# Optimization experiments

Hardware: AMD Instinct MI355X
Metric: run time of the kernel (lower is better)

## Reference

```python
import jax, jax.numpy as jnp
import numpy as np

B = 64
E = 512          # latent_size / h_dim
H = 8            # num_heads
D = E // H       # head_dim
MAX_AGENTS = 254 # max(agents_per_sample) for the deterministic counts below
NEG = -1e9


def setup_inputs() -> dict:
    key = jax.random.key(0)
    k_x, k_wi, k_bi, k_wo, k_bo = jax.random.split(key, 5)
    # deterministic variable agent counts in [128, 254]; sum == 11531, max == 254
    agents = jnp.array([128 + (3 * i) % 129 for i in range(B)], dtype=jnp.int32)
    total = 11531
    att_in = jax.random.normal(k_x, (total, E), dtype=jnp.float32)
    # nn.MultiheadAttention params: packed in-proj [3E, E] + bias, out-proj [E, E] + bias
    w_in = jax.random.normal(k_wi, (3 * E, E), dtype=jnp.float32) * 0.02
    b_in = jax.random.normal(k_bi, (3 * E,), dtype=jnp.float32) * 0.02
    w_out = jax.random.normal(k_wo, (E, E), dtype=jnp.float32) * 0.02
    b_out = jax.random.normal(k_bo, (E,), dtype=jnp.float32) * 0.02
    return {"att_in": att_in, "w_in": w_in, "b_in": b_in,
            "w_out": w_out, "b_out": b_out, "agents_per_sample": agents}


def reference(att_in, w_in, b_in, w_out, b_out, agents_per_sample):
    S = MAX_AGENTS
    # scatter packed rows into padded [B, S, E] via a clipped gather (jit-safe)
    offsets = jnp.cumsum(agents_per_sample) - agents_per_sample      # [B]
    pos = jnp.arange(S, dtype=jnp.int32)
    mask = pos[None, :] < agents_per_sample[:, None]                 # [B, S] valid
    idx = jnp.clip(offsets[:, None] + pos[None, :], 0, att_in.shape[0] - 1)
    padded = jnp.where(mask[..., None], att_in[idx], 0.0)            # [B, S, E]

    # fused QKV projection (torch packed in_proj), dropout disabled (eval)
    qkv = padded @ w_in.T + b_in                                     # [B, S, 3E]
    q, k, v = jnp.split(qkv, 3, axis=-1)
    q = q.reshape(B, S, H, D)
    k = k.reshape(B, S, H, D)
    v = v.reshape(B, S, H, D)

    scores = jnp.einsum('bqhd,bkhd->bhqk', q, k) * (D ** -0.5)      # [B, H, S, S]
    scores = jnp.where(mask[:, None, None, :], scores, NEG)          # key_padding_mask
    attn = jax.nn.softmax(scores, axis=-1)
    ctx = jnp.einsum('bhqk,bkhd->bqhd', attn, v).reshape(B, S, E)
    out = ctx @ w_out.T + b_out                                      # [B, S, E]
    # torch returns only valid rows per sample; zero the padded rows instead
    return out * mask[..., None]
```

## Files before the change

### kernel.cpp

```cpp
#include <hip/hip_runtime.h>
#include <hip/hip_bf16.h>

typedef __attribute__((ext_vector_type(8))) short bf16x8;
typedef __attribute__((ext_vector_type(4))) float f32x4;
typedef __attribute__((ext_vector_type(4))) int i32x4;
typedef __attribute__((ext_vector_type(4))) unsigned short u16x4;
typedef __attribute__((ext_vector_type(2))) unsigned ui2;
typedef __attribute__((ext_vector_type(4))) float fl4;

struct __attribute__((packed)) u16x4u { u16x4 v; };

__device__ __forceinline__ f32x4 mfma16(bf16x8 a, bf16x8 b, f32x4 c) {
    return __builtin_amdgcn_mfma_f32_16x16x32_bf16(a, b, c, 0, 0, 0);
}

__device__ __forceinline__ unsigned short f2b(float f) {
    unsigned u = __float_as_uint(f);
    unsigned r = (u + 0x7FFF + ((u >> 16) & 1)) >> 16;
    return (unsigned short)r;
}

__device__ __forceinline__ int bsearch_off(const int* s_off, int m) {
    int lo = 0, hi = 63;
    while (lo < hi) {
        int mid = (lo + hi + 1) >> 1;
        if (s_off[mid] <= m) lo = mid; else hi = mid - 1;
    }
    return lo;
}

__device__ __forceinline__ void gld_lds16(const __hip_bfloat16* g, __hip_bfloat16* l) {
    __builtin_amdgcn_global_load_lds(
        (const __attribute__((address_space(1))) void*)g,
        (__attribute__((address_space(3))) void*)l,
        16, 0, 0);
}

__global__ void k_prep(const unsigned short* __restrict__ src,
                       const void* __restrict__ b_in, const void* __restrict__ b_out,
                       const int* __restrict__ agents,
                       int* __restrict__ flag, int* __restrict__ offs,
                       float* __restrict__ bfi, float* __restrict__ bfo) {
    __shared__ int sh[256];
    __shared__ int sa[64];
    __shared__ int sflag;
    int tid = threadIdx.x;
    int h = 0;
    for (int i = tid; i < 16384; i += 256) {
        unsigned e = (src[i] >> 7) & 0xFF;
        if (e == 0xFF) h = 1;
    }
    sh[tid] = h;
    if (tid < 64) sa[tid] = agents[tid];
    __syncthreads();
    if (tid < 64) {
        int v = sh[tid] | sh[tid + 64] | sh[tid + 128] | sh[tid + 192];
        unsigned long long m = __ballot(v != 0);
        if (tid == 0) { flag[0] = (m != 0) ? 1 : 0; sflag = (m != 0) ? 1 : 0; }
        int ex = 0;
        for (int i = 0; i < 64; ++i) { int w = sa[i]; if (i < tid) ex += w; }
        offs[tid] = ex;
        if (tid == 63) offs[64] = ex + sa[63];
    }
    __syncthreads();
    int f = sflag;
    for (int i = tid; i < 1536; i += 256)
        bfi[i] = f ? ((const float*)b_in)[i]
                   : __bfloat162float(((const __hip_bfloat16*)b_in)[i]);
    for (int i = tid; i < 512; i += 256)
        bfo[i] = f ? ((const float*)b_out)[i]
                   : __bfloat162float(((const __hip_bfloat16*)b_out)[i]);
}

__global__ void k_cast_all(const void* __restrict__ sA, unsigned short* __restrict__ dA, int nA,
                           const void* __restrict__ sWi, unsigned short* __restrict__ dWi, int nWi,
                           const void* __restrict__ sWo, unsigned short* __restrict__ dWo, int nWo,
                           const int* __restrict__ flag) {
    int i = (blockIdx.x * 256 + threadIdx.x) * 4;
    const void* src; unsigned short* dst; int k;
    if (i < nA)            { src = sA;  dst = dA;  k = i; }
    else if (i < nA + nWi) { src = sWi; dst = dWi; k = i - nA; }
    else if (i < nA + nWi + nWo) { src = sWo; dst = dWo; k = i - nA - nWi; }
    else return;
    u16x4 o;
    if (flag[0]) {
        fl4 v = *(const fl4*)((const float*)src + k);
        o[0] = f2b(v[0]); o[1] = f2b(v[1]); o[2] = f2b(v[2]); o[3] = f2b(v[3]);
    } else {
        o = *(const u16x4*)((const unsigned short*)src + k);
    }
    *(u16x4*)(dst + k) = o;
}

template<int LDA, bool MROWS>
__device__ __forceinline__ void gemm_core(
    const __hip_bfloat16* __restrict__ A,
    const __hip_bfloat16* __restrict__ W,
    int m0, int n0, int total,
    __hip_bfloat16* As, __hip_bfloat16* Ws,
    f32x4 acc[4][4], int tid)
{
    int lane = tid & 63, quad = lane >> 4, c = lane & 15;
    int wave = tid >> 6;
    int wr = wave >> 1, wc = wave & 1;

    const __hip_bfloat16* gA[4];
    const __hip_bfloat16* gW[4];
    __hip_bfloat16* lA[4];
    __hip_bfloat16* lW[4];
#pragma unroll
    for (int j = 0; j < 4; ++j) {
        int L = j * 256 + tid;
        int row = L >> 3;
        int gseg = (L & 7) ^ (row & 7);
        int ar = m0 + row; if (ar > total - 1) ar = total - 1;
        gA[j] = A + (size_t)ar * LDA + gseg * 8;
        gW[j] = W + (size_t)(n0 + row) * 512 + gseg * 8;
        lA[j] = As + (size_t)(j * 256 + wave * 64) * 8;
        lW[j] = Ws + (size_t)(j * 256 + wave * 64) * 8;
    }

#pragma unroll
    for (int j = 0; j < 4; ++j) gld_lds16(gA[j], lA[j]);
#pragma unroll
    for (int j = 0; j < 4; ++j) gld_lds16(gW[j], lW[j]);

#pragma unroll
    for (int s = 0; s < 8; ++s) {
        const int cur = s & 1;
        const int nxt = cur ^ 1;
        if (s < 7) {
            int k0 = (s + 1) * 64;
#pragma unroll
            for (int j = 0; j < 4; ++j) gld_lds16(gA[j] + k0, lA[j] + nxt * (128 * 64));
#pragma unroll
            for (int j = 0; j < 4; ++j) gld_lds16(gW[j] + k0, lW[j] + nxt * (128 * 64));
            asm volatile("s_waitcnt vmcnt(8)" ::: "memory");
        } else {
            asm volatile("s_waitcnt vmcnt(0)" ::: "memory");
        }
        __builtin_amdgcn_s_barrier();
        const __hip_bfloat16* Ab = As + cur * (128 * 64);
        const __hip_bfloat16* Wb = Ws + cur * (128 * 64);
#pragma unroll
        for (int h = 0; h < 2; ++h) {
            bf16x8 af[4], wf[4];
#pragma unroll
            for (int t = 0; t < 4; ++t) {
                int rowa = wr * 64 + t * 16 + c;
                int rowb = wc * 64 + t * 16 + c;
                int ks = quad + 4 * h;
                af[t] = *(const bf16x8*)(Ab + (size_t)rowa * 64 + ((ks ^ (rowa & 7)) * 8));
                wf[t] = *(const bf16x8*)(Wb + (size_t)rowb * 64 + ((ks ^ (rowb & 7)) * 8));
            }
#pragma unroll
            for (int i = 0; i < 4; ++i)
#pragma unroll
                for (int j = 0; j < 4; ++j)
                    acc[i][j] = MROWS ? mfma16(af[i], wf[j], acc[i][j])
                                      : mfma16(wf[j], af[i], acc[i][j]);
        }
        if (s < 7) __builtin_amdgcn_s_barrier();
    }
}

template<bool MROWS>
__device__ __forceinline__ void gemm256_core(
    const __hip_bfloat16* __restrict__ A,
    const __hip_bfloat16* __restrict__ W,
    int m0, int n0, int total,
    __hip_bfloat16* As, __hip_bfloat16* Ws,
    f32x4 acc[8][4], int tid)
{
    int lane = tid & 63, quad = lane >> 4, c = lane & 15;
    int wave = tid >> 6;
    int wm = wave >> 2, wn = wave & 3;

    const __hip_bfloat16* gA[4];
    const __hip_bfloat16* gW[4];
    __hip_bfloat16* lA[4];
    __hip_bfloat16* lW[4];
#pragma unroll
    for (int j = 0; j < 4; ++j) {
        int L = j * 512 + tid;
        int row = L >> 3;
        int gseg = (L & 7) ^ (row & 7);
        int ar = m0 + row; if (ar > total - 1) ar = total - 1;
        gA[j] = A + (size_t)ar * 512 + gseg * 8;
        gW[j] = W + (size_t)(n0 + row) * 512 + gseg * 8;
        lA[j] = As + (size_t)(j * 512 + wave * 64) * 8;
        lW[j] = Ws + (size_t)(j * 512 + wave * 64) * 8;
    }

#pragma unroll
    for (int j = 0; j < 4; ++j) gld_lds16(gA[j], lA[j]);
#pragma unroll
    for (int j = 0; j < 4; ++j) gld_lds16(gW[j], lW[j]);

#pragma unroll
    for (int s = 0; s < 8; ++s) {
        const int cur = s & 1;
        const int nxt = cur ^ 1;
        if (s < 7) {
            int k0 = (s + 1) * 64;
#pragma unroll
            for (int j = 0; j < 4; ++j) gld_lds16(gA[j] + k0, lA[j] + nxt * (256 * 64));
#pragma unroll
            for (int j = 0; j < 4; ++j) gld_lds16(gW[j] + k0, lW[j] + nxt * (256 * 64));
            asm volatile("s_waitcnt vmcnt(8)" ::: "memory");
        } else {
            asm volatile("s_waitcnt vmcnt(0)" ::: "memory");
        }
        __builtin_amdgcn_s_barrier();
        const __hip_bfloat16* Ab = As + cur * (256 * 64);
        const __hip_bfloat16* Wb = Ws + cur * (256 * 64);
#pragma unroll
        for (int h = 0; h < 2; ++h) {
            bf16x8 af[8], wf[4];
            int ks = quad + 4 * h;
#pragma unroll
            for (int t = 0; t < 8; ++t) {
                int rowa = wm * 128 + t * 16 + c;
                af[t] = *(const bf16x8*)(Ab + (size_t)rowa * 64 + ((ks ^ (rowa & 7)) * 8));
            }
#pragma unroll
            for (int t = 0; t < 4; ++t) {
                int rowb = wn * 64 + t * 16 + c;
                wf[t] = *(const bf16x8*)(Wb + (size_t)rowb * 64 + ((ks ^ (rowb & 7)) * 8));
            }
#pragma unroll
            for (int i = 0; i < 8; ++i)
#pragma unroll
                for (int j = 0; j < 4; ++j)
                    acc[i][j] = MROWS ? mfma16(af[i], wf[j], acc[i][j])
                                      : mfma16(wf[j], af[i], acc[i][j]);
        }
        if (s < 7) __builtin_amdgcn_s_barrier();
    }
}

__global__ __launch_bounds__(512, 2) void k_qkv(
    const __hip_bfloat16* __restrict__ A,
    const __hip_bfloat16* __restrict__ W,
    const float* __restrict__ bias,
    const int* __restrict__ offs,
    __hip_bfloat16* __restrict__ qP,
    __hip_bfloat16* __restrict__ kP,
    __hip_bfloat16* __restrict__ vT,
    int total)
{
    __shared__ __hip_bfloat16 As[2 * 256 * 64];
    __shared__ __hip_bfloat16 Ws[2 * 256 * 64];
    __shared__ int s_off[65];
    int l = blockIdx.x;
    int rb = l / 6;
    int cb = l - rb * 6;
    int n0 = cb * 256;
    int m0 = rb * 256;
    int tid = threadIdx.x;
    if (tid < 65) s_off[tid] = offs[tid];
    int lane = tid & 63, quad = lane >> 4, c = lane & 15;
    int wave = tid >> 6, wm = wave >> 2, wn = wave & 3;
    f32x4 z = {0.f, 0.f, 0.f, 0.f};
    f32x4 acc[8][4] = {{z,z,z,z},{z,z,z,z},{z,z,z,z},{z,z,z,z},
                       {z,z,z,z},{z,z,z,z},{z,z,z,z},{z,z,z,z}};

    if (n0 < 1024) {
        gemm256_core<false>(A, W, m0, n0, total, As, Ws, acc, tid);
        __hip_bfloat16* dst = (n0 < 512) ? qP : kP;
        int nb = n0 & 511;
        int head = (nb + wn * 64) >> 6;
        fl4 bv4[4];
#pragma unroll
        for (int j = 0; j < 4; ++j)
            bv4[j] = *(const fl4*)&bias[n0 + wn * 64 + j * 16 + quad * 4];
#pragma unroll
        for (int i = 0; i < 8; ++i) {
            int m = m0 + wm * 128 + i * 16 + c;
            if (m >= total) continue;
            int lo = bsearch_off(s_off, m);
            int vs = m - s_off[lo];
            size_t rowp = ((size_t)(lo * 8 + head) * 256 + vs) * 64;
#pragma unroll
            for (int j = 0; j < 4; ++j) {
                int dcol = j * 16 + quad * 4;
                u16x4 o;
#pragma unroll
                for (int r = 0; r < 4; ++r) o[r] = f2b(acc[i][j][r] + bv4[j][r]);
                *(u16x4*)&dst[rowp + dcol] = o;
            }
        }
    } else {
        gemm256_core<true>(A, W, m0, n0, total, As, Ws, acc, tid);
        float bv[4];
#pragma unroll
        for (int j = 0; j < 4; ++j) bv[j] = bias[n0 + wn * 64 + j * 16 + c];
#pragma unroll
        for (int i = 0; i < 8; ++i) {
            int m_base = m0 + wm * 128 + i * 16 + quad * 4;
            if (m_base >= total) continue;
            int lo = bsearch_off(s_off, m_base);
            bool vec = (m_base + 3 < total) && (s_off[lo + 1] > m_base + 3);
            if (vec) {
                int vs = m_base - s_off[lo];
#pragma unroll
                for (int j = 0; j < 4; ++j) {
                    int vc = n0 - 1024 + wn * 64 + j * 16 + c;
                    size_t idx = ((size_t)(lo * 8 + (vc >> 6)) * 64 + (vc & 63)) * 256 + vs;
                    u16x4 o;
#pragma unroll
                    for (int r = 0; r < 4; ++r) o[r] = f2b(acc[i][j][r] + bv[j]);
                    ((u16x4u*)&vT[idx])->v = o;
                }
            } else {
#pragma unroll
                for (int r = 0; r < 4; ++r) {
                    int m = m_base + r;
                    if (m >= total) continue;
                    int lo2 = bsearch_off(s_off, m);
                    int vs2 = m - s_off[lo2];
#pragma unroll
                    for (int j = 0; j < 4; ++j) {
                        int vc = n0 - 1024 + wn * 64 + j * 16 + c;
                        vT[((size_t)(lo2 * 8 + (vc >> 6)) * 64 + (vc & 63)) * 256 + vs2] =
                            __float2bfloat16(acc[i][j][r] + bv[j]);
                    }
                }
            }
        }
    }
}

__global__ __launch_bounds__(256, 2) void k_attn(
    const __hip_bfloat16* __restrict__ qP,
    const __hip_bfloat16* __restrict__ kP,
    const __hip_bfloat16* __restrict__ vT,
    __hip_bfloat16* __restrict__ ctx,
    const int* __restrict__ agents,
    const int* __restrict__ offs)
{
    __shared__ __attribute__((aligned(16))) char Pl[4][16 * 80];
    int bh = blockIdx.x;
    int b = bh >> 3, h = bh & 7;
    int n = agents[b];
    int off = offs[b];
    int qtiles = (n + 15) >> 4;
    int stmax = (qtiles + 1) >> 1;
    int tid = threadIdx.x;
    int wave = tid >> 6, lane = tid & 63, quad = lane >> 4, c = lane & 15;
    const __hip_bfloat16* qbase = qP + (size_t)bh * 256 * 64;
    const __hip_bfloat16* kbase = kP + (size_t)bh * 256 * 64 + quad * 8;
    const __hip_bfloat16* vbase = vT + (size_t)bh * 64 * 256;
    char* Plw = &Pl[wave][0];

    bf16x8 qB[4][2];
    int nt = 0;
#pragma unroll
    for (int t = 0; t < 4; ++t) {
        int qt = wave + 4 * t;
        if (qt < qtiles) {
            nt = t + 1;
            int qr = qt * 16 + c; if (qr > n - 1) qr = n - 1;
            const __hip_bfloat16* qp = qbase + (size_t)qr * 64 + quad * 8;
            qB[t][0] = *(const bf16x8*)qp;
            qB[t][1] = *(const bf16x8*)(qp + 32);
        }
    }

    f32x4 z = {0.f, 0.f, 0.f, 0.f};
    f32x4 O[4][4] = {{z,z,z,z},{z,z,z,z},{z,z,z,z},{z,z,z,z}};
    float sm[4] = {0.f, 0.f, 0.f, 0.f};

    auto LK = [&](int st, bf16x8 kA[2][2], bf16x8 vA[4]) {
        int k0 = st * 32;
#pragma unroll
        for (int ti = 0; ti < 2; ++ti) {
            int kr = k0 + ti * 16 + c; if (kr > n - 1) kr = n - 1;
            const __hip_bfloat16* kp = kbase + (size_t)kr * 64;
            kA[ti][0] = *(const bf16x8*)kp;
            kA[ti][1] = *(const bf16x8*)(kp + 32);
        }
#pragma unroll
        for (int dt = 0; dt < 4; ++dt)
            vA[dt] = *(const bf16x8*)(vbase + (size_t)(dt * 16 + c) * 256 + k0 + quad * 8);
    };

    auto CMP = [&](int st, bf16x8 kA[2][2], bf16x8 vA[4]) {
        int k0 = st * 32;
#pragma unroll
        for (int t = 0; t < 4; ++t) {
            if (t < nt) {
#pragma unroll
                for (int ti = 0; ti < 2; ++ti) {
                    f32x4 s = mfma16(kA[ti][0], qB[t][0], z);
                    s = mfma16(kA[ti][1], qB[t][1], s);
                    int kbase_i = k0 + ti * 16 + quad * 4;
                    float p0 = (kbase_i + 0 < n) ? __expf(s[0] * 0.125f) : 0.f;
                    float p1 = (kbase_i + 1 < n) ? __expf(s[1] * 0.125f) : 0.f;
                    float p2 = (kbase_i + 2 < n) ? __expf(s[2] * 0.125f) : 0.f;
                    float p3 = (kbase_i + 3 < n) ? __expf(s[3] * 0.125f) : 0.f;
                    sm[t] += (p0 + p1) + (p2 + p3);
                    ui2 dw;
                    dw[0] = (unsigned)f2b(p0) | ((unsigned)f2b(p1) << 16);
                    dw[1] = (unsigned)f2b(p2) | ((unsigned)f2b(p3) << 16);
                    *(ui2*)(Plw + c * 80 + ti * 32 + quad * 8) = dw;
                }
                bf16x8 pB = *(const bf16x8*)(Plw + c * 80 + quad * 16);
#pragma unroll
                for (int dt = 0; dt < 4; ++dt)
                    O[t][dt] = mfma16(vA[dt], pB, O[t][dt]);
            }
        }
    };

    bf16x8 kA[2][2], vA[4], kB[2][2], vB[4], kC[2][2], vC[4];
    LK(0, kA, vA);
    if (1 < stmax) LK(1, kB, vB);
    for (int st = 0; st < stmax; st += 3) {
        if (st + 2 < stmax) LK(st + 2, kC, vC);
        CMP(st, kA, vA);
        if (st + 3 < stmax) LK(st + 3, kA, vA);
        if (st + 1 < stmax) CMP(st + 1, kB, vB);
        if (st + 4 < stmax) LK(st + 4, kB, vB);
        if (st + 2 < stmax) CMP(st + 2, kC, vC);
    }

#pragma unroll
    for (int t = 0; t < 4; ++t) {
        if (t < nt) {
            float v = sm[t];
            v += __shfl_xor(v, 16);
            v += __shfl_xor(v, 32);
            float iv = 1.0f / v;
            int q = (wave + 4 * t) * 16 + c;
            if (q < n) {
                size_t row = (size_t)(off + q) * 512 + h * 64;
#pragma unroll
                for (int dt = 0; dt < 4; ++dt) {
                    u16x4 o;
#pragma unroll
                    for (int r = 0; r < 4; ++r) o[r] = f2b(O[t][dt][r] * iv);
                    *(u16x4*)&ctx[row + dt * 16 + quad * 4] = o;
                }
            }
        }
    }
}

__global__ __launch_bounds__(256) void k_out(
    const __hip_bfloat16* __restrict__ A,
    const __hip_bfloat16* __restrict__ W,
    const float* __restrict__ bias,
    const int* __restrict__ offs,
    const int* __restrict__ agents,
    void* __restrict__ out,
    const int* __restrict__ flag,
    int total, int MT)
{
    __shared__ __hip_bfloat16 As[2 * 128 * 64];
    __shared__ __hip_bfloat16 Ws[2 * 128 * 64];
    __shared__ int s_off[65];
    int l = blockIdx.x;
    int MTpad = ((MT + 7) >> 3) << 3;
    int tid = threadIdx.x;
    if (l >= 4 * MTpad) {
        int b = l - 4 * MTpad;
        int n = agents[b];
        int esz = flag[0] ? 4 : 2;
        long long base = ((long long)b * 254 + n) * 512 * esz;
        long long bytes = (long long)(254 - n) * 512 * esz;
        for (long long i = (long long)tid * 16; i < bytes; i += (long long)256 * 16)
            *(i32x4*)((char*)out + base + i) = (i32x4){0, 0, 0, 0};
        return;
    }
    int inner = l >> 3;
    int cb = inner & 3;
    int rb = (l & 7) + 8 * (inner >> 2);
    if (rb >= MT) return;
    int n0 = cb * 128;
    int m0 = rb * 128;
    if (tid < 65) s_off[tid] = offs[tid];
    f32x4 z = {0.f, 0.f, 0.f, 0.f};
    f32x4 acc[4][4] = {{z,z,z,z},{z,z,z,z},{z,z,z,z},{z,z,z,z}};
    gemm_core<512, false>(A, W, m0, n0, total, As, Ws, acc, tid);

    int f32m = flag[0];
    int lane = tid & 63, quad = lane >> 4, c = lane & 15;
    int wave = tid >> 6, wr = wave >> 1, wc = wave & 1;
    fl4 bv4[4];
#pragma unroll
    for (int j = 0; j < 4; ++j)
        bv4[j] = *(const fl4*)&bias[n0 + wc * 64 + j * 16 + quad * 4];
#pragma unroll
    for (int i = 0; i < 4; ++i) {
        int m = m0 + wr * 64 + i * 16 + c;
        if (m >= total) continue;
        int lo = bsearch_off(s_off, m);
        int os_ = m - s_off[lo];
        size_t rowb = ((size_t)(lo * 254 + os_)) * 512;
#pragma unroll
        for (int j = 0; j < 4; ++j) {
            int col0 = n0 + wc * 64 + j * 16 + quad * 4;
            if (f32m) {
                fl4 o;
#pragma unroll
                for (int r = 0; r < 4; ++r) o[r] = acc[i][j][r] + bv4[j][r];
                *(fl4*)&((float*)out)[rowb + col0] = o;
            } else {
                u16x4 o;
#pragma unroll
                for (int r = 0; r < 4; ++r) o[r] = f2b(acc[i][j][r] + bv4[j][r]);
                *(u16x4*)&((__hip_bfloat16*)out)[rowb + col0] = o;
            }
        }
    }
}

extern "C" void kernel_launch(void* const* d_in, const int* in_sizes, int n_in,
                              void* d_out, int out_size, void* d_ws, size_t ws_size,
                              hipStream_t stream) {
    const void* att_in = d_in[0];
    const void* w_in   = d_in[1];
    const void* b_in   = d_in[2];
    const void* w_out  = d_in[3];
    const void* b_out  = d_in[4];
    const int* agents  = (const int*)d_in[5];
    int total = in_sizes[0] / 512;

    char* p = (char*)d_ws;
    int* flag  = (int*)p;                 p += 256;
    int* offs  = (int*)p;                 p += 512;
    float* bfi = (float*)p;               p += 1536 * 4;
    float* bfo = (float*)p;               p += 512 * 4;
    __hip_bfloat16* WinBf  = (__hip_bfloat16*)p;  p += (size_t)1536 * 512 * 2;
    __hip_bfloat16* WoutBf = (__hip_bfloat16*)p;  p += (size_t)512 * 512 * 2;
    __hip_bfloat16* Abf    = (__hip_bfloat16*)p;  p += (size_t)total * 512 * 2;
    __hip_bfloat16* qP     = (__hip_bfloat16*)p;  p += (size_t)512 * 256 * 64 * 2;
    __hip_bfloat16* kP     = (__hip_bfloat16*)p;  p += (size_t)512 * 256 * 64 * 2;
    __hip_bfloat16* vT     = (__hip_bfloat16*)p;  p += (size_t)512 * 64 * 256 * 2;
    __hip_bfloat16* ctx    = (__hip_bfloat16*)p;  p += (size_t)total * 512 * 2;

    int nA = total * 512, nWi = 1536 * 512, nWo = 512 * 512;
    int ntot = nA + nWi + nWo;

    k_prep<<<1, 256, 0, stream>>>((const unsigned short*)att_in, b_in, b_out,
                                  agents, flag, offs, bfi, bfo);
    k_cast_all<<<(ntot / 4 + 255) / 256, 256, 0, stream>>>(
        att_in, (unsigned short*)Abf, nA,
        w_in,   (unsigned short*)WinBf, nWi,
        w_out,  (unsigned short*)WoutBf, nWo, flag);

    int MT = (total + 127) / 128;
    int MTpad = ((MT + 7) / 8) * 8;
    int MT256 = (total + 255) / 256;
    k_qkv<<<6 * MT256, 512, 0, stream>>>(Abf, WinBf, bfi, offs, qP, kP, vT, total);
    k_attn<<<512, 256, 0, stream>>>(qP, kP, vT, ctx, agents, offs);
    k_out<<<4 * MTpad + 64, 256, 0, stream>>>(ctx, WoutBf, bfo, offs, agents,
                                              d_out, flag, total, MT);
}
```

Measured before the change: 190.2 us.

## Split QKV GEMM K-step into two phases, remap XCD blocks, widen out-proj to 8 waves

```diff
diff --git a/kernel.cpp b/kernel.cpp
--- a/kernel.cpp
+++ b/kernel.cpp
@@ -98,32 +98,32 @@
     const __hip_bfloat16* __restrict__ W,
     int m0, int n0, int total,
     __hip_bfloat16* As, __hip_bfloat16* Ws,
-    f32x4 acc[4][4], int tid)
+    f32x4 acc[4][2], int tid)
 {
     int lane = tid & 63, quad = lane >> 4, c = lane & 15;
     int wave = tid >> 6;
-    int wr = wave >> 1, wc = wave & 1;
-
-    const __hip_bfloat16* gA[4];
-    const __hip_bfloat16* gW[4];
-    __hip_bfloat16* lA[4];
-    __hip_bfloat16* lW[4];
-#pragma unroll
-    for (int j = 0; j < 4; ++j) {
-        int L = j * 256 + tid;
+    int wm = wave >> 2, wn = wave & 3;
+
+    const __hip_bfloat16* gA[2];
+    const __hip_bfloat16* gW[2];
+    __hip_bfloat16* lA[2];
+    __hip_bfloat16* lW[2];
+#pragma unroll
+    for (int j = 0; j < 2; ++j) {
+        int L = j * 512 + tid;
         int row = L >> 3;
         int gseg = (L & 7) ^ (row & 7);
         int ar = m0 + row; if (ar > total - 1) ar = total - 1;
         gA[j] = A + (size_t)ar * LDA + gseg * 8;
         gW[j] = W + (size_t)(n0 + row) * 512 + gseg * 8;
-        lA[j] = As + (size_t)(j * 256 + wave * 64) * 8;
-        lW[j] = Ws + (size_t)(j * 256 + wave * 64) * 8;
-    }
-
-#pragma unroll
-    for (int j = 0; j < 4; ++j) gld_lds16(gA[j], lA[j]);
-#pragma unroll
-    for (int j = 0; j < 4; ++j) gld_lds16(gW[j], lW[j]);
+        lA[j] = As + (size_t)(j * 512 + wave * 64) * 8;
+        lW[j] = Ws + (size_t)(j * 512 + wave * 64) * 8;
+    }
+
+#pragma unroll
+    for (int j = 0; j < 2; ++j) gld_lds16(gA[j], lA[j]);
+#pragma unroll
+    for (int j = 0; j < 2; ++j) gld_lds16(gW[j], lW[j]);
 
 #pragma unroll
     for (int s = 0; s < 8; ++s) {
@@ -132,10 +132,10 @@
         if (s < 7) {
             int k0 = (s + 1) * 64;
 #pragma unroll
-            for (int j = 0; j < 4; ++j) gld_lds16(gA[j] + k0, lA[j] + nxt * (128 * 64));
-#pragma unroll
-            for (int j = 0; j < 4; ++j) gld_lds16(gW[j] + k0, lW[j] + nxt * (128 * 64));
-            asm volatile("s_waitcnt vmcnt(8)" ::: "memory");
+            for (int j = 0; j < 2; ++j) gld_lds16(gA[j] + k0, lA[j] + nxt * (128 * 64));
+#pragma unroll
+            for (int j = 0; j < 2; ++j) gld_lds16(gW[j] + k0, lW[j] + nxt * (128 * 64));
+            asm volatile("s_waitcnt vmcnt(4)" ::: "memory");
         } else {
             asm volatile("s_waitcnt vmcnt(0)" ::: "memory");
         }
@@ -144,19 +144,22 @@
         const __hip_bfloat16* Wb = Ws + cur * (128 * 64);
 #pragma unroll
         for (int h = 0; h < 2; ++h) {
-            bf16x8 af[4], wf[4];
+            bf16x8 af[4], wf[2];
+            int ks = quad + 4 * h;
 #pragma unroll
             for (int t = 0; t < 4; ++t) {
-                int rowa = wr * 64 + t * 16 + c;
-                int rowb = wc * 64 + t * 16 + c;
-                int ks = quad + 4 * h;
+                int rowa = wm * 64 + t * 16 + c;
                 af[t] = *(const bf16x8*)(Ab + (size_t)rowa * 64 + ((ks ^ (rowa & 7)) * 8));
+            }
+#pragma unroll
+            for (int t = 0; t < 2; ++t) {
+                int rowb = wn * 32 + t * 16 + c;
                 wf[t] = *(const bf16x8*)(Wb + (size_t)rowb * 64 + ((ks ^ (rowb & 7)) * 8));
             }
 #pragma unroll
             for (int i = 0; i < 4; ++i)
 #pragma unroll
-                for (int j = 0; j < 4; ++j)
+                for (int j = 0; j < 2; ++j)
                     acc[i][j] = MROWS ? mfma16(af[i], wf[j], acc[i][j])
                                       : mfma16(wf[j], af[i], acc[i][j]);
         }
@@ -201,41 +204,52 @@
     for (int s = 0; s < 8; ++s) {
         const int cur = s & 1;
         const int nxt = cur ^ 1;
-        if (s < 7) {
-            int k0 = (s + 1) * 64;
-#pragma unroll
-            for (int j = 0; j < 4; ++j) gld_lds16(gA[j] + k0, lA[j] + nxt * (256 * 64));
-#pragma unroll
-            for (int j = 0; j < 4; ++j) gld_lds16(gW[j] + k0, lW[j] + nxt * (256 * 64));
-            asm volatile("s_waitcnt vmcnt(8)" ::: "memory");
-        } else {
-            asm volatile("s_waitcnt vmcnt(0)" ::: "memory");
-        }
-        __builtin_amdgcn_s_barrier();
         const __hip_bfloat16* Ab = As + cur * (256 * 64);
         const __hip_bfloat16* Wb = Ws + cur * (256 * 64);
 #pragma unroll
-        for (int h = 0; h < 2; ++h) {
-            bf16x8 af[8], wf[4];
-            int ks = quad + 4 * h;
-#pragma unroll
-            for (int t = 0; t < 8; ++t) {
-                int rowa = wm * 128 + t * 16 + c;
-                af[t] = *(const bf16x8*)(Ab + (size_t)rowa * 64 + ((ks ^ (rowa & 7)) * 8));
-            }
-#pragma unroll
-            for (int t = 0; t < 4; ++t) {
-                int rowb = wn * 64 + t * 16 + c;
-                wf[t] = *(const bf16x8*)(Wb + (size_t)rowb * 64 + ((ks ^ (rowb & 7)) * 8));
-            }
-#pragma unroll
-            for (int i = 0; i < 8; ++i)
-#pragma unroll
-                for (int j = 0; j < 4; ++j)
-                    acc[i][j] = MROWS ? mfma16(af[i], wf[j], acc[i][j])
-                                      : mfma16(wf[j], af[i], acc[i][j]);
-        }
-        if (s < 7) __builtin_amdgcn_s_barrier();
+        for (int ph = 0; ph < 2; ++ph) {
+            if (ph == 0)      asm volatile("s_waitcnt vmcnt(2)" ::: "memory");
+            else if (s < 7)   asm volatile("s_waitcnt vmcnt(6)" ::: "memory");
+            else              asm volatile("s_waitcnt vmcnt(0)" ::: "memory");
+            __builtin_amdgcn_s_barrier();
+            if (s < 7) {
+                int k0 = (s + 1) * 64;
+                if (ph == 0) {
+#pragma unroll
+                    for (int j = 0; j < 4; ++j) gld_lds16(gA[j] + k0, lA[j] + nxt * (256 * 64));
+#pragma unroll
+                    for (int j = 0; j < 2; ++j) gld_lds16(gW[j] + k0, lW[j] + nxt * (256 * 64));
+                } else {
+#pragma unroll
+                    for (int j = 2; j < 4; ++j) gld_lds16(gW[j] + k0, lW[j] + nxt * (256 * 64));
+                }
+            }
+#pragma unroll
+            for (int h = 0; h < 2; ++h) {
+                int ks = quad + 4 * h;
+                bf16x8 af[8], wf[2];
+#pragma unroll
+                for (int t = 0; t < 8; ++t) {
+                    int rowa = wm * 128 + t * 16 + c;
+                    af[t] = *(const bf16x8*)(Ab + (size_t)rowa * 64 + ((ks ^ (rowa & 7)) * 8));
+                }
+#pragma unroll
+                for (int t = 0; t < 2; ++t) {
+                    int rowb = ph * 128 + wn * 32 + t * 16 + c;
+                    wf[t] = *(const bf16x8*)(Wb + (size_t)rowb * 64 + ((ks ^ (rowb & 7)) * 8));
+                }
+                __builtin_amdgcn_s_setprio(1);
+#pragma unroll
+                for (int i = 0; i < 8; ++i)
+#pragma unroll
+                    for (int j = 0; j < 2; ++j) {
+                        int jj = ph * 2 + j;
+                        acc[i][jj] = MROWS ? mfma16(af[i], wf[j], acc[i][jj])
+                                           : mfma16(wf[j], af[i], acc[i][jj]);
+                    }
+                __builtin_amdgcn_s_setprio(0);
+            }
+        }
     }
 }
 
@@ -252,9 +266,13 @@
     __shared__ __hip_bfloat16 As[2 * 256 * 64];
     __shared__ __hip_bfloat16 Ws[2 * 256 * 64];
     __shared__ int s_off[65];
-    int l = blockIdx.x;
-    int rb = l / 6;
-    int cb = l - rb * 6;
+    int nwg = gridDim.x;
+    int bid = blockIdx.x;
+    int xcd = bid & 7, idx = bid >> 3;
+    int q = nwg >> 3, r = nwg & 7;
+    int wg = (xcd < r ? xcd * (q + 1) : r * (q + 1) + (xcd - r) * q) + idx;
+    int rb = wg / 6;
+    int cb = wg - rb * 6;
     int n0 = cb * 256;
     int m0 = rb * 256;
     int tid = threadIdx.x;
@@ -269,24 +287,25 @@
         gemm256_core<false>(A, W, m0, n0, total, As, Ws, acc, tid);
         __hip_bfloat16* dst = (n0 < 512) ? qP : kP;
         int nb = n0 & 511;
-        int head = (nb + wn * 64) >> 6;
         fl4 bv4[4];
 #pragma unroll
-        for (int j = 0; j < 4; ++j)
-            bv4[j] = *(const fl4*)&bias[n0 + wn * 64 + j * 16 + quad * 4];
+        for (int jj = 0; jj < 4; ++jj)
+            bv4[jj] = *(const fl4*)&bias[n0 + (jj >> 1) * 128 + wn * 32 + (jj & 1) * 16 + quad * 4];
 #pragma unroll
         for (int i = 0; i < 8; ++i) {
             int m = m0 + wm * 128 + i * 16 + c;
             if (m >= total) continue;
             int lo = bsearch_off(s_off, m);
             int vs = m - s_off[lo];
-            size_t rowp = ((size_t)(lo * 8 + head) * 256 + vs) * 64;
-#pragma unroll
-            for (int j = 0; j < 4; ++j) {
-                int dcol = j * 16 + quad * 4;
+#pragma unroll
+            for (int jj = 0; jj < 4; ++jj) {
+                int ch = jj >> 1, j2 = jj & 1;
+                int head = (nb >> 6) + ch * 2 + (wn >> 1);
+                int dcol = (wn & 1) * 32 + j2 * 16 + quad * 4;
+                size_t rowp = ((size_t)(lo * 8 + head) * 256 + vs) * 64;
                 u16x4 o;
 #pragma unroll
-                for (int r = 0; r < 4; ++r) o[r] = f2b(acc[i][j][r] + bv4[j][r]);
+                for (int r2 = 0; r2 < 4; ++r2) o[r2] = f2b(acc[i][jj][r2] + bv4[jj][r2]);
                 *(u16x4*)&dst[rowp + dcol] = o;
             }
         }
@@ -294,7 +313,8 @@
         gemm256_core<true>(A, W, m0, n0, total, As, Ws, acc, tid);
         float bv[4];
 #pragma unroll
-        for (int j = 0; j < 4; ++j) bv[j] = bias[n0 + wn * 64 + j * 16 + c];
+        for (int jj = 0; jj < 4; ++jj)
+            bv[jj] = bias[n0 + (jj >> 1) * 128 + wn * 32 + (jj & 1) * 16 + c];
 #pragma unroll
         for (int i = 0; i < 8; ++i) {
             int m_base = m0 + wm * 128 + i * 16 + quad * 4;
@@ -304,26 +324,26 @@
             if (vec) {
                 int vs = m_base - s_off[lo];
 #pragma unroll
-                for (int j = 0; j < 4; ++j) {
-                    int vc = n0 - 1024 + wn * 64 + j * 16 + c;
-                    size_t idx = ((size_t)(lo * 8 + (vc >> 6)) * 64 + (vc & 63)) * 256 + vs;
+                for (int jj = 0; jj < 4; ++jj) {
+                    int vc = n0 - 1024 + (jj >> 1) * 128 + wn * 32 + (jj & 1) * 16 + c;
+                    size_t idxv = ((size_t)(lo * 8 + (vc >> 6)) * 64 + (vc & 63)) * 256 + vs;
                     u16x4 o;
 #pragma unroll
-                    for (int r = 0; r < 4; ++r) o[r] = f2b(acc[i][j][r] + bv[j]);
-                    ((u16x4u*)&vT[idx])->v = o;
+                    for (int r2 = 0; r2 < 4; ++r2) o[r2] = f2b(acc[i][jj][r2] + bv[jj]);
+                    ((u16x4u*)&vT[idxv])->v = o;
                 }
             } else {
 #pragma unroll
-                for (int r = 0; r < 4; ++r) {
-                    int m = m_base + r;
+                for (int r2 = 0; r2 < 4; ++r2) {
+                    int m = m_base + r2;
                     if (m >= total) continue;
                     int lo2 = bsearch_off(s_off, m);
                     int vs2 = m - s_off[lo2];
 #pragma unroll
-                    for (int j = 0; j < 4; ++j) {
-                        int vc = n0 - 1024 + wn * 64 + j * 16 + c;
+                    for (int jj = 0; jj < 4; ++jj) {
+                        int vc = n0 - 1024 + (jj >> 1) * 128 + wn * 32 + (jj & 1) * 16 + c;
                         vT[((size_t)(lo2 * 8 + (vc >> 6)) * 64 + (vc & 63)) * 256 + vs2] =
-                            __float2bfloat16(acc[i][j][r] + bv[j]);
+                            __float2bfloat16(acc[i][jj][r2] + bv[jj]);
                     }
                 }
             }
@@ -447,7 +467,7 @@
     }
 }
 
-__global__ __launch_bounds__(256) void k_out(
+__global__ __launch_bounds__(512, 4) void k_out(
     const __hip_bfloat16* __restrict__ A,
     const __hip_bfloat16* __restrict__ W,
     const float* __restrict__ bias,
@@ -469,7 +489,7 @@
         int esz = flag[0] ? 4 : 2;
         long long base = ((long long)b * 254 + n) * 512 * esz;
         long long bytes = (long long)(254 - n) * 512 * esz;
-        for (long long i = (long long)tid * 16; i < bytes; i += (long long)256 * 16)
+        for (long long i = (long long)tid * 16; i < bytes; i += (long long)512 * 16)
             *(i32x4*)((char*)out + base + i) = (i32x4){0, 0, 0, 0};
         return;
     }
@@ -481,26 +501,26 @@
     int m0 = rb * 128;
     if (tid < 65) s_off[tid] = offs[tid];
     f32x4 z = {0.f, 0.f, 0.f, 0.f};
-    f32x4 acc[4][4] = {{z,z,z,z},{z,z,z,z},{z,z,z,z},{z,z,z,z}};
+    f32x4 acc[4][2] = {{z,z},{z,z},{z,z},{z,z}};
     gemm_core<512, false>(A, W, m0, n0, total, As, Ws, acc, tid);
 
     int f32m = flag[0];
     int lane = tid & 63, quad = lane >> 4, c = lane & 15;
-    int wave = tid >> 6, wr = wave >> 1, wc = wave & 1;
-    fl4 bv4[4];
-#pragma unroll
-    for (int j = 0; j < 4; ++j)
-        bv4[j] = *(const fl4*)&bias[n0 + wc * 64 + j * 16 + quad * 4];
+    int wave = tid >> 6, wm = wave >> 2, wn = wave & 3;
+    fl4 bv4[2];
+#pragma unroll
+    for (int j = 0; j < 2; ++j)
+        bv4[j] = *(const fl4*)&bias[n0 + wn * 32 + j * 16 + quad * 4];
 #pragma unroll
     for (int i = 0; i < 4; ++i) {
-        int m = m0 + wr * 64 + i * 16 + c;
+        int m = m0 + wm * 64 + i * 16 + c;
         if (m >= total) continue;
         int lo = bsearch_off(s_off, m);
         int os_ = m - s_off[lo];
         size_t rowb = ((size_t)(lo * 254 + os_)) * 512;
 #pragma unroll
-        for (int j = 0; j < 4; ++j) {
-            int col0 = n0 + wc * 64 + j * 16 + quad * 4;
+        for (int j = 0; j < 2; ++j) {
+            int col0 = n0 + wn * 32 + j * 16 + quad * 4;
             if (f32m) {
                 fl4 o;
 #pragma unroll
@@ -555,6 +575,6 @@
     int MT256 = (total + 255) / 256;
     k_qkv<<<6 * MT256, 512, 0, stream>>>(Abf, WinBf, bfi, offs, qP, kP, vT, total);
     k_attn<<<512, 256, 0, stream>>>(qP, kP, vT, ctx, agents, offs);
-    k_out<<<4 * MTpad + 64, 256, 0, stream>>>(ctx, WoutBf, bfo, offs, agents,
+    k_out<<<4 * MTpad + 64, 512, 0, stream>>>(ctx, WoutBf, bfo, offs, agents,
                                               d_out, flag, total, MT);
 }
```

Measured after the change: 190.8 us. About the same (+0.3%).
